# Performance work log

Hardware: AMD Instinct MI355X
Metric: run time of the kernel (lower is better)

The kernel has to match this reference:

```python
import jax, jax.numpy as jnp
import numpy as np

B, S, D_IN, D_OUT = 4, 4096, 1024, 1024

def setup_inputs() -> dict:
    key = jax.random.key(0)
    kx, kq, kk, kv = jax.random.split(key, 4)
    x = jax.random.normal(kx, (B, S, D_IN), dtype=jnp.float32)
    # torch nn.Linear stores weight as [d_out, d_in]; y = x @ W.T
    Wq = jax.random.normal(kq, (D_OUT, D_IN), dtype=jnp.float32) * 0.02
    Wk = jax.random.normal(kk, (D_OUT, D_IN), dtype=jnp.float32) * 0.02
    Wv = jax.random.normal(kv, (D_OUT, D_IN), dtype=jnp.float32) * 0.02
    return {"x": x, "Wq": Wq, "Wk": Wk, "Wv": Wv}

def reference(x, Wq, Wk, Wv):
    b, n, _ = x.shape
    d_out = Wk.shape[0]
    q = jnp.einsum('bnd,od->bno', x, Wq)
    k = jnp.einsum('bnd,od->bno', x, Wk)
    v = jnp.einsum('bnd,od->bno', x, Wv)
    scores = jnp.einsum('bqo,bko->bqk', q, k)  # [B, S, S]
    causal = jnp.triu(jnp.ones((n, n), dtype=bool), k=1)
    scores = jnp.where(causal, -jnp.inf, scores)
    attn = jax.nn.softmax(scores / jnp.sqrt(jnp.float32(d_out)), axis=-1)
    # dropout p=0.0 -> identity
    return jnp.einsum('bqk,bko->bqo', attn, v)
```

## Files before the change

### kernel.cpp

```cpp
#include <hip/hip_runtime.h>


typedef unsigned short u16;
typedef unsigned int u32;
typedef __attribute__((ext_vector_type(8))) short bf16x8;
typedef __attribute__((ext_vector_type(4))) float f32x4;
typedef __attribute__((ext_vector_type(8))) unsigned short u16x8;

__device__ __forceinline__ u16 f2bf(float f) {
  union { float f; unsigned u; } v; v.f = f;
  unsigned r = v.u + 0x7FFFu + ((v.u >> 16) & 1u);
  return (u16)(r >> 16);
}
__device__ __forceinline__ float bf2f(u16 h) {
  union { unsigned u; float f; } v; v.u = ((unsigned)h) << 16;
  return v.f;
}
__device__ __forceinline__ f32x4 mfma16(bf16x8 a, bf16x8 b, f32x4 c) {
  return __builtin_amdgcn_mfma_f32_16x16x32_bf16(a, b, c, 0, 0, 0);
}
__device__ __forceinline__ void gld_lds16(const u16* g, u16* l) {
  __builtin_amdgcn_global_load_lds(
      (const __attribute__((address_space(1))) u32*)g,
      (__attribute__((address_space(3))) u32*)l, 16, 0, 0);
}

__global__ __launch_bounds__(256)
void cast_f32_bf16(const float* __restrict__ src, u16* __restrict__ dst, int n8) {
  int i = blockIdx.x * 256 + threadIdx.x;
  if (i >= n8) return;
  const float4* s4 = (const float4*)src;
  float4 a = s4[2*i], b = s4[2*i+1];
  u16x8 o;
  o[0]=f2bf(a.x); o[1]=f2bf(a.y); o[2]=f2bf(a.z); o[3]=f2bf(a.w);
  o[4]=f2bf(b.x); o[5]=f2bf(b.y); o[6]=f2bf(b.z); o[7]=f2bf(b.w);
  ((u16x8*)dst)[i] = o;
}

__global__ __launch_bounds__(512)
void qkv_gemm(const u16* __restrict__ X, const u16* __restrict__ W,
              u16* __restrict__ Qo, u16* __restrict__ Ko, u16* __restrict__ VTo) {
  __shared__ __align__(16) u16 At[2][256 * 64];
  __shared__ __align__(16) u16 Bt[2][256 * 64];
  const int tid = threadIdx.x;
  const int w = tid >> 6, lane = tid & 63;
  const int g = lane >> 4, c16 = lane & 15;
  const int wr = w >> 2, wc = w & 3;
  const int M0 = blockIdx.x * 256;
  const int N0 = blockIdx.y * 256;

  f32x4 acc[8][4] = {};

  auto stage = [&](int s, int k0) {
#pragma unroll
    for (int i = 0; i < 4; ++i) {
      int ci = i * 512 + tid;
      int r = ci >> 3;
      int c = (ci & 7) ^ (r & 7);
      gld_lds16(X + (size_t)(M0 + r) * 1024 + k0 + c * 8, &At[s][ci * 8]);
    }
#pragma unroll
    for (int i = 0; i < 4; ++i) {
      int ci = i * 512 + tid;
      int r = ci >> 3;
      int c = (ci & 7) ^ (r & 7);
      gld_lds16(W + (size_t)(N0 + r) * 1024 + k0 + c * 8, &Bt[s][ci * 8]);
    }
  };
  auto compute = [&](int s) {
#pragma unroll
    for (int dk = 0; dk < 2; ++dk) {
      bf16x8 af[8], bfr[4];
#pragma unroll
      for (int m = 0; m < 8; ++m) {
        int row = wr * 128 + m * 16 + c16;
        int ch = dk * 4 + g;
        af[m] = *(const bf16x8*)&At[s][row * 64 + ((ch ^ (row & 7)) * 8)];
      }
#pragma unroll
      for (int n = 0; n < 4; ++n) {
        int row = wc * 64 + n * 16 + c16;
        int ch = dk * 4 + g;
        bfr[n] = *(const bf16x8*)&Bt[s][row * 64 + ((ch ^ (row & 7)) * 8)];
      }
#pragma unroll
      for (int m = 0; m < 8; ++m)
#pragma unroll
        for (int n = 0; n < 4; ++n)
          acc[m][n] = mfma16(af[m], bfr[n], acc[m][n]);
    }
  };

  stage(0, 0);
  __syncthreads();
  int cur = 0;
  for (int t = 0; t < 16; ++t) {
    if (t < 15) stage(cur ^ 1, (t + 1) * 64);
    compute(cur);
    __syncthreads();
    cur ^= 1;
  }

  const int which = N0 >> 10;
  const int colbase = N0 & 1023;
#pragma unroll
  for (int m = 0; m < 8; ++m) {
#pragma unroll
    for (int n = 0; n < 4; ++n) {
#pragma unroll
      for (int r = 0; r < 4; ++r) {
        int gm  = M0 + wr * 128 + m * 16 + 4 * g + r;
        int col = colbase + wc * 64 + n * 16 + c16;
        u16 hv = f2bf(acc[m][n][r]);
        if (which == 0) {
          Qo[(size_t)gm * 1024 + col] = hv;
        } else if (which == 1) {
          Ko[(size_t)gm * 1024 + col] = hv;
        } else {
          int b = gm >> 12, s = gm & 4095;
          VTo[((size_t)((b << 10) + col)) * 4096 + s] = hv;
        }
      }
    }
  }
}

__global__ __launch_bounds__(512)
void sgemm_exp(const u16* __restrict__ Q, const u16* __restrict__ K,
               u16* __restrict__ Spack, float* __restrict__ lpart) {
  __shared__ __align__(16) u16 At[2][256 * 64];
  __shared__ __align__(16) u16 Bt[2][256 * 64];
  __shared__ float lsum[256][4];
  const int tid = threadIdx.x;
  const int w = tid >> 6, lane = tid & 63;
  const int g = lane >> 4, c16 = lane & 15;
  const int wr = w >> 2, wc = w & 3;
  const int b = blockIdx.y;

  int L = blockIdx.x, qt = 0;
  while ((qt + 1) * (qt + 2) / 2 <= L) ++qt;
  const int kt = L - qt * (qt + 1) / 2;

  const u16* Qb = Q + (size_t)b * 4096 * 1024 + (size_t)qt * 256 * 1024;
  const u16* Kb = K + (size_t)b * 4096 * 1024 + (size_t)kt * 256 * 1024;

  f32x4 acc[8][4] = {};

  auto stage = [&](int s, int k0) {
#pragma unroll
    for (int i = 0; i < 4; ++i) {
      int ci = i * 512 + tid;
      int r = ci >> 3;
      int c = (ci & 7) ^ (r & 7);
      gld_lds16(Qb + (size_t)r * 1024 + k0 + c * 8, &At[s][ci * 8]);
    }
#pragma unroll
    for (int i = 0; i < 4; ++i) {
      int ci = i * 512 + tid;
      int r = ci >> 3;
      int c = (ci & 7) ^ (r & 7);
      gld_lds16(Kb + (size_t)r * 1024 + k0 + c * 8, &Bt[s][ci * 8]);
    }
  };
  auto compute = [&](int s) {
#pragma unroll
    for (int dk = 0; dk < 2; ++dk) {
      bf16x8 af[8], bfr[4];
#pragma unroll
      for (int m = 0; m < 8; ++m) {
        int row = wr * 128 + m * 16 + c16;
        int ch = dk * 4 + g;
        af[m] = *(const bf16x8*)&At[s][row * 64 + ((ch ^ (row & 7)) * 8)];
      }
#pragma unroll
      for (int n = 0; n < 4; ++n) {
        int row = wc * 64 + n * 16 + c16;
        int ch = dk * 4 + g;
        bfr[n] = *(const bf16x8*)&Bt[s][row * 64 + ((ch ^ (row & 7)) * 8)];
      }
#pragma unroll
      for (int m = 0; m < 8; ++m)
#pragma unroll
        for (int n = 0; n < 4; ++n)
          acc[m][n] = mfma16(af[m], bfr[n], acc[m][n]);
    }
  };

  stage(0, 0);
  __syncthreads();
  int cur = 0;
  for (int t = 0; t < 16; ++t) {
    if (t < 15) stage(cur ^ 1, (t + 1) * 64);
    compute(cur);
    __syncthreads();
    cur ^= 1;
  }

  const int qt128 = 2 * qt + wr;
  const int kt128 = 2 * kt + (wc >> 1);
  const bool exists = (kt128 <= qt128);
  u16* Sb = Spack + (((size_t)b * 528 + (size_t)(qt128 * (qt128 + 1)) / 2 + kt128) << 14);
  const int q0 = qt * 256, k0g = kt * 256;
  float psum[8][4];
#pragma unroll
  for (int m = 0; m < 8; ++m)
#pragma unroll
    for (int r = 0; r < 4; ++r) psum[m][r] = 0.f;
#pragma unroll
  for (int m = 0; m < 8; ++m) {
#pragma unroll
    for (int n = 0; n < 4; ++n) {
#pragma unroll
      for (int r = 0; r < 4; ++r) {
        int rl = wr * 128 + m * 16 + 4 * g + r;
        int cl = wc * 64 + n * 16 + c16;
        float s = acc[m][n][r] * 0.03125f;
        float p = (k0g + cl <= q0 + rl) ? __expf(s) : 0.f;
        u16 pb = f2bf(p);
        if (exists) Sb[(rl & 127) * 128 + (cl & 127)] = pb;
        psum[m][r] += bf2f(pb);
      }
    }
  }
#pragma unroll
  for (int m = 0; m < 8; ++m)
#pragma unroll
    for (int r = 0; r < 4; ++r) {
      float v = psum[m][r];
      v += __shfl_xor(v, 1, 64);
      v += __shfl_xor(v, 2, 64);
      v += __shfl_xor(v, 4, 64);
      v += __shfl_xor(v, 8, 64);
      psum[m][r] = v;
    }
  if (c16 == 0) {
#pragma unroll
    for (int m = 0; m < 8; ++m)
#pragma unroll
      for (int r = 0; r < 4; ++r)
        lsum[wr * 128 + m * 16 + 4 * g + r][wc] = psum[m][r];
  }
  __syncthreads();
  if (tid < 256) {
    float v = lsum[tid][0] + lsum[tid][1] + lsum[tid][2] + lsum[tid][3];
    lpart[((size_t)b * 4096 + q0 + tid) * 16 + kt] = v;
  }
}

__global__ __launch_bounds__(256)
void lreduce(const float* __restrict__ lpart, float* __restrict__ linv) {
  int row = blockIdx.x * 256 + threadIdx.x;
  int nt  = ((row & 4095) >> 8) + 1;
  const float* p = lpart + (size_t)row * 16;
  float s = 0.f;
  for (int i = 0; i < nt; ++i) s += p[i];
  linv[row] = 1.f / s;
}

__global__ __launch_bounds__(512)
void pv_gemm(const u16* __restrict__ Spack, const u16* __restrict__ VT,
             const u16* __restrict__ ztile, const float* __restrict__ linv,
             float* __restrict__ Out) {
  __shared__ __align__(16) u16 At[2][256 * 64];
  __shared__ __align__(16) u16 Bt[2][128 * 64];
  const int tid = threadIdx.x;
  const int w = tid >> 6, lane = tid & 63;
  const int g = lane >> 4, c16 = lane & 15;
  const int wm = w >> 1, wn = w & 1;
  const int p  = blockIdx.x;
  const int d0 = blockIdx.y;
  const int b  = blockIdx.z;

  const u16* Sp_b = Spack + (size_t)b * 528 * 16384;
  const u16* VTb  = VT + (size_t)b * 1024 * 4096;
  float* Ob = Out + (size_t)b * 4096 * 1024;

  for (int pass = 0; pass < 2; ++pass) {
    const int QT = pass == 0 ? p : 15 - p;
    const int M0 = QT * 256;
    const int nsteps = (QT + 1) * 4;
    const int tLo = 2 * QT;
    const size_t triLo = (size_t)(tLo * (tLo + 1)) / 2;
    const size_t triHi = (size_t)((tLo + 1) * (tLo + 2)) / 2;

    f32x4 acc[4][4] = {};

    auto stage = [&](int s, int tt) {
      const int kv0 = tt * 64;
      const int kt128 = tt >> 1;
      const int koff = (tt & 1) * 64;
      const u16* baseLo = (kt128 <= tLo) ? Sp_b + ((triLo + kt128) << 14) : ztile;
      const u16* baseHi = Sp_b + ((triHi + kt128) << 14);
#pragma unroll
      for (int i = 0; i < 4; ++i) {
        int ci = i * 512 + tid;
        int r = ci >> 3;
        int c = (ci & 7) ^ (r & 7);
        const u16* base = (i < 2) ? baseLo : baseHi;
        gld_lds16(base + (size_t)(r & 127) * 128 + koff + c * 8, &At[s][ci * 8]);
      }
#pragma unroll
      for (int i = 0; i < 2; ++i) {
        int ci = i * 512 + tid;
        int r = ci >> 3;
        int c = (ci & 7) ^ (r & 7);
        gld_lds16(VTb + (size_t)(d0 * 128 + r) * 4096 + kv0 + c * 8, &Bt[s][ci * 8]);
      }
    };
    auto compute = [&](int s) {
#pragma unroll
      for (int dk = 0; dk < 2; ++dk) {
        bf16x8 af[4], bfr[4];
#pragma unroll
        for (int m = 0; m < 4; ++m) {
          int row = wm * 64 + m * 16 + c16;
          int ch = dk * 4 + g;
          af[m] = *(const bf16x8*)&At[s][row * 64 + ((ch ^ (row & 7)) * 8)];
        }
#pragma unroll
        for (int n = 0; n < 4; ++n) {
          int row = wn * 64 + n * 16 + c16;
          int ch = dk * 4 + g;
          bfr[n] = *(const bf16x8*)&Bt[s][row * 64 + ((ch ^ (row & 7)) * 8)];
        }
#pragma unroll
        for (int m = 0; m < 4; ++m)
#pragma unroll
          for (int n = 0; n < 4; ++n)
            acc[m][n] = mfma16(af[m], bfr[n], acc[m][n]);
      }
    };

    stage(0, 0);
    __syncthreads();
    int cur = 0;
    for (int t = 0; t < nsteps; ++t) {
      if (t + 1 < nsteps) stage(cur ^ 1, t + 1);
      compute(cur);
      __syncthreads();
      cur ^= 1;
    }

    const float* lb = linv + (size_t)b * 4096 + M0;
#pragma unroll
    for (int m = 0; m < 4; ++m) {
#pragma unroll
      for (int r = 0; r < 4; ++r) {
        int rl = wm * 64 + m * 16 + 4 * g + r;
        float li = lb[rl];
#pragma unroll
        for (int n = 0; n < 4; ++n) {
          int dcol = d0 * 128 + wn * 64 + n * 16 + c16;
          Ob[(size_t)(M0 + rl) * 1024 + dcol] = acc[m][n][r] * li;
        }
      }
    }
  }
}

__global__ __launch_bounds__(512, 2)
void attn_kernel(const u16* __restrict__ Q, const u16* __restrict__ K,
                 const u16* __restrict__ VT, float* __restrict__ Out) {
  __shared__ u16 kv_lds[32 * 1024];
  __shared__ float s_part[4][32][33];
  __shared__ u16 p_lds[32 * 40];
  __shared__ float l_lds[32];

  const int tid = threadIdx.x;
  const int w = tid >> 6, lane = tid & 63;
  const int g = lane >> 4, c16 = lane & 15;
  const int b  = blockIdx.x & 3;
  const int qb = 127 - (blockIdx.x >> 2);
  const int qs = qb * 32;
  const int kh = w & 1, dq = w >> 1;

  const u16* Qb  = Q  + (size_t)b * 4096 * 1024;
  const u16* Kb  = K  + (size_t)b * 4096 * 1024;
  const u16* VTb = VT + (size_t)b * 1024 * 4096;

  bf16x8 qfrag[2][8];
#pragma unroll
  for (int qh = 0; qh < 2; ++qh)
#pragma unroll
    for (int dk = 0; dk < 8; ++dk)
      qfrag[qh][dk] = *(const bf16x8*)(Qb + (size_t)(qs + qh * 16 + c16) * 1024
                                       + dq * 256 + dk * 32 + g * 8);

  f32x4 oacc[2][8] = {};
  if (tid < 32) l_lds[tid] = 0.f;

  const int qrow_p = tid >> 4;
  const int kk     = tid & 15;
  const int gq     = qs + qrow_p;

  for (int j = 0; j <= qb; ++j) {
    const int kv0 = j * 32;
    __syncthreads();
    uint4 rk[8];
#pragma unroll
    for (int i = 0; i < 8; ++i) {
      int ci = i * 512 + tid;
      int r  = ci >> 7;
      int c  = (ci & 127) ^ (r & 7);
      rk[i] = *(const uint4*)(Kb + (size_t)(kv0 + r) * 1024 + c * 8);
    }
#pragma unroll
    for (int i = 0; i < 8; ++i)
      *(uint4*)&kv_lds[(size_t)(i * 512 + tid) * 8] = rk[i];
    __syncthreads();
    f32x4 sacc[2] = {};
#pragma unroll
    for (int dk = 0; dk < 8; ++dk) {
      int kvrow = kh * 16 + c16;
      int ch    = dq * 32 + dk * 4 + g;
      bf16x8 kf = *(const bf16x8*)&kv_lds[kvrow * 1024 + ((ch ^ (kvrow & 7)) * 8)];
      sacc[0] = mfma16(qfrag[0][dk], kf, sacc[0]);
      sacc[1] = mfma16(qfrag[1][dk], kf, sacc[1]);
    }
#pragma unroll
    for (int qh = 0; qh < 2; ++qh)
#pragma unroll
      for (int r = 0; r < 4; ++r)
        s_part[dq][qh * 16 + 4 * g + r][kh * 16 + c16] = sacc[qh][r];
    __syncthreads();
    uint4 rv[8];
#pragma unroll
    for (int i = 0; i < 8; ++i) {
      int ci = i * 512 + tid;
      int d  = ((ci >> 6) << 4) + (ci & 15);
      int c  = (ci >> 4) & 3;
      rv[i] = *(const uint4*)(VTb + (size_t)d * 4096 + kv0 + c * 8);
    }
    {
      float psum = 0.f;
#pragma unroll
      for (int h = 0; h < 2; ++h) {
        int kcol = kk + h * 16;
        float s = s_part[0][qrow_p][kcol] + s_part[1][qrow_p][kcol]
                + s_part[2][qrow_p][kcol] + s_part[3][qrow_p][kcol];
        s *= 0.03125f;
        float p = (kv0 + kcol <= gq) ? __expf(s) : 0.f;
        u16 pb = f2bf(p);
        p_lds[qrow_p * 40 + kcol] = pb;
        psum += bf2f(pb);
      }
#pragma unroll
      for (int off = 1; off < 16; off <<= 1)
        psum += __shfl_xor(psum, off, 64);
      if (kk == 0) l_lds[qrow_p] += psum;
    }
#pragma unroll
    for (int i = 0; i < 8; ++i)
      *(uint4*)&kv_lds[(size_t)(i * 512 + tid) * 8] = rv[i];
    __syncthreads();
    bf16x8 pa0 = *(const bf16x8*)&p_lds[(0  + c16) * 40 + g * 8];
    bf16x8 pa1 = *(const bf16x8*)&p_lds[(16 + c16) * 40 + g * 8];
#pragma unroll
    for (int f = 0; f < 8; ++f) {
      int dcol = w * 128 + f * 16 + c16;
      int pos  = (dcol >> 4) * 64 + g * 16 + (dcol & 15);
      bf16x8 vf = *(const bf16x8*)&kv_lds[(size_t)pos * 8];
      oacc[0][f] = mfma16(pa0, vf, oacc[0][f]);
      oacc[1][f] = mfma16(pa1, vf, oacc[1][f]);
    }
  }

  float* Ob = Out + (size_t)b * 4096 * 1024;
#pragma unroll
  for (int qh = 0; qh < 2; ++qh) {
#pragma unroll
    for (int r = 0; r < 4; ++r) {
      int ql = qh * 16 + 4 * g + r;
      float linvv = 1.f / l_lds[ql];
#pragma unroll
      for (int f = 0; f < 8; ++f)
        Ob[(size_t)(qs + ql) * 1024 + w * 128 + f * 16 + c16] = oacc[qh][f][r] * linvv;
    }
  }
}

extern "C" void kernel_launch(void* const* d_in, const int* in_sizes, int n_in,
                              void* d_out, int out_size, void* d_ws, size_t ws_size,
                              hipStream_t stream) {
  const float* x  = (const float*)d_in[0];
  const float* Wq = (const float*)d_in[1];
  const float* Wk = (const float*)d_in[2];
  const float* Wv = (const float*)d_in[3];
  float* out = (float*)d_out;

  u16* ws    = (u16*)d_ws;
  u16* wWqkv = ws;
  u16* wX    = wWqkv + (size_t)3 * 1024 * 1024;
  u16* wQ    = wX + (size_t)16384 * 1024;
  u16* wK    = wQ + (size_t)16384 * 1024;
  u16* wVT   = wK + (size_t)16384 * 1024;
  u16* wSp   = wVT + (size_t)16384 * 1024;
  float* lpart = (float*)(ws + (size_t)104857600);
  float* linv  = (float*)(ws + (size_t)105906176);

  cast_f32_bf16<<<dim3(8192), 256, 0, stream>>>(x, wX, 16777216 / 8);
  cast_f32_bf16<<<dim3(512), 256, 0, stream>>>(Wq, wWqkv,                 1048576 / 8);
  cast_f32_bf16<<<dim3(512), 256, 0, stream>>>(Wk, wWqkv + 1048576,       1048576 / 8);
  cast_f32_bf16<<<dim3(512), 256, 0, stream>>>(Wv, wWqkv + 2 * 1048576,   1048576 / 8);

  qkv_gemm<<<dim3(64, 12), 512, 0, stream>>>(wX, wWqkv, wQ, wK, wVT);

  if (ws_size >= (size_t)211877888) {
    hipMemsetAsync(wX, 0, 32768, stream);
    sgemm_exp<<<dim3(136, 4), 512, 0, stream>>>(wQ, wK, wSp, lpart);
    lreduce<<<dim3(64), 256, 0, stream>>>(lpart, linv);
    pv_gemm<<<dim3(8, 8, 4), 512, 0, stream>>>(wSp, wVT, wX, linv, out);
  } else {
    attn_kernel<<<dim3(512), 512, 0, stream>>>(wQ, wK, wVT, out);
  }
}
```

Baseline: 393.6 us.

## Use 4-stage 32-wide K pipeline with fragment-ordered LDS layout in GEMMs

Replaces the double-buffered 64-wide K stages in all three GEMM kernels with a 4-slot ring of 32-wide K stages. Each slot is laid out in MFMA-fragment order with an XOR swizzle, so each fragment read is a single contiguous vector load. Partial vmcnt waits let three stages of global-to-LDS loads stay in flight, and s_setprio raises wave priority around the MFMA block. This is meant to hide memory latency better, at the cost of twice as many barriers per K and hand-tuned vmcnt counts that must match the number of loads issued.

```diff
diff --git a/kernel.cpp b/kernel.cpp
--- a/kernel.cpp
+++ b/kernel.cpp
@@ -40,8 +40,8 @@
 __global__ __launch_bounds__(512)
 void qkv_gemm(const u16* __restrict__ X, const u16* __restrict__ W,
               u16* __restrict__ Qo, u16* __restrict__ Ko, u16* __restrict__ VTo) {
-  __shared__ __align__(16) u16 At[2][256 * 64];
-  __shared__ __align__(16) u16 Bt[2][256 * 64];
+  __shared__ __align__(16) u16 LA[4][8192];
+  __shared__ __align__(16) u16 LB[4][8192];
   const int tid = threadIdx.x;
   const int w = tid >> 6, lane = tid & 63;
   const int g = lane >> 4, c16 = lane & 15;
@@ -50,55 +50,61 @@
   const int N0 = blockIdx.y * 256;
 
   f32x4 acc[8][4] = {};
-
-  auto stage = [&](int s, int k0) {
-#pragma unroll
-    for (int i = 0; i < 4; ++i) {
-      int ci = i * 512 + tid;
-      int r = ci >> 3;
-      int c = (ci & 7) ^ (r & 7);
-      gld_lds16(X + (size_t)(M0 + r) * 1024 + k0 + c * 8, &At[s][ci * 8]);
-    }
-#pragma unroll
-    for (int i = 0; i < 4; ++i) {
-      int ci = i * 512 + tid;
-      int r = ci >> 3;
-      int c = (ci & 7) ^ (r & 7);
-      gld_lds16(W + (size_t)(N0 + r) * 1024 + k0 + c * 8, &Bt[s][ci * 8]);
+  const int roff = c16 * 32 + ((g ^ (c16 & 3)) * 8);
+
+  auto stage = [&](int s) {
+    const int slot = s & 3;
+    const int k0 = s * 32;
+#pragma unroll
+    for (int i = 0; i < 2; ++i) {
+      int p = i * 512 + tid;
+      int r = ((p >> 6) << 4) | ((p >> 2) & 15);
+      int c = (p & 3) ^ ((p >> 2) & 3);
+      gld_lds16(X + (size_t)(M0 + r) * 1024 + k0 + c * 8, &LA[slot][p * 8]);
+    }
+#pragma unroll
+    for (int i = 0; i < 2; ++i) {
+      int p = i * 512 + tid;
+      int r = ((p >> 6) << 4) | ((p >> 2) & 15);
+      int c = (p & 3) ^ ((p >> 2) & 3);
+      gld_lds16(W + (size_t)(N0 + r) * 1024 + k0 + c * 8, &LB[slot][p * 8]);
     }
   };
-  auto compute = [&](int s) {
-#pragma unroll
-    for (int dk = 0; dk < 2; ++dk) {
-      bf16x8 af[8], bfr[4];
-#pragma unroll
-      for (int m = 0; m < 8; ++m) {
-        int row = wr * 128 + m * 16 + c16;
-        int ch = dk * 4 + g;
-        af[m] = *(const bf16x8*)&At[s][row * 64 + ((ch ^ (row & 7)) * 8)];
-      }
-#pragma unroll
-      for (int n = 0; n < 4; ++n) {
-        int row = wc * 64 + n * 16 + c16;
-        int ch = dk * 4 + g;
-        bfr[n] = *(const bf16x8*)&Bt[s][row * 64 + ((ch ^ (row & 7)) * 8)];
-      }
+
+  stage(0); stage(1); stage(2);
+  for (int s = 0; s < 32; ++s) {
+    if (s + 3 < 32) {
+      stage(s + 3);
+      asm volatile("s_waitcnt vmcnt(12)" ::: "memory");
+    } else {
+      asm volatile("s_waitcnt vmcnt(0)" ::: "memory");
+    }
+    __builtin_amdgcn_sched_barrier(0);
+    __builtin_amdgcn_s_barrier();
+    __builtin_amdgcn_sched_barrier(0);
+    {
+      const int slot = s & 3;
+      const u16* A = LA[slot];
+      const u16* B = LB[slot];
+      bf16x8 af[8], bf[4];
 #pragma unroll
       for (int m = 0; m < 8; ++m)
+        af[m] = *(const bf16x8*)&A[(wr * 8 + m) * 512 + roff];
+#pragma unroll
+      for (int n = 0; n < 4; ++n)
+        bf[n] = *(const bf16x8*)&B[(wc * 4 + n) * 512 + roff];
+      __builtin_amdgcn_s_setprio(1);
+#pragma unroll
+      for (int m = 0; m < 8; ++m)
 #pragma unroll
         for (int n = 0; n < 4; ++n)
-          acc[m][n] = mfma16(af[m], bfr[n], acc[m][n]);
-    }
-  };
-
-  stage(0, 0);
-  __syncthreads();
-  int cur = 0;
-  for (int t = 0; t < 16; ++t) {
-    if (t < 15) stage(cur ^ 1, (t + 1) * 64);
-    compute(cur);
-    __syncthreads();
-    cur ^= 1;
+          acc[m][n] = mfma16(af[m], bf[n], acc[m][n]);
+      __builtin_amdgcn_s_setprio(0);
+    }
+    asm volatile("s_waitcnt lgkmcnt(0)" ::: "memory");
+    __builtin_amdgcn_sched_barrier(0);
+    __builtin_amdgcn_s_barrier();
+    __builtin_amdgcn_sched_barrier(0);
   }
 
   const int which = N0 >> 10;
@@ -117,8 +123,8 @@
         } else if (which == 1) {
           Ko[(size_t)gm * 1024 + col] = hv;
         } else {
-          int b = gm >> 12, s = gm & 4095;
-          VTo[((size_t)((b << 10) + col)) * 4096 + s] = hv;
+          int b = gm >> 12, s2 = gm & 4095;
+          VTo[((size_t)((b << 10) + col)) * 4096 + s2] = hv;
         }
       }
     }
@@ -128,8 +134,8 @@
 __global__ __launch_bounds__(512)
 void sgemm_exp(const u16* __restrict__ Q, const u16* __restrict__ K,
                u16* __restrict__ Spack, float* __restrict__ lpart) {
-  __shared__ __align__(16) u16 At[2][256 * 64];
-  __shared__ __align__(16) u16 Bt[2][256 * 64];
+  __shared__ __align__(16) u16 LA[4][8192];
+  __shared__ __align__(16) u16 LB[4][8192];
   __shared__ float lsum[256][4];
   const int tid = threadIdx.x;
   const int w = tid >> 6, lane = tid & 63;
@@ -145,55 +151,61 @@
   const u16* Kb = K + (size_t)b * 4096 * 1024 + (size_t)kt * 256 * 1024;
 
   f32x4 acc[8][4] = {};
-
-  auto stage = [&](int s, int k0) {
-#pragma unroll
-    for (int i = 0; i < 4; ++i) {
-      int ci = i * 512 + tid;
-      int r = ci >> 3;
-      int c = (ci & 7) ^ (r & 7);
-      gld_lds16(Qb + (size_t)r * 1024 + k0 + c * 8, &At[s][ci * 8]);
-    }
-#pragma unroll
-    for (int i = 0; i < 4; ++i) {
-      int ci = i * 512 + tid;
-      int r = ci >> 3;
-      int c = (ci & 7) ^ (r & 7);
-      gld_lds16(Kb + (size_t)r * 1024 + k0 + c * 8, &Bt[s][ci * 8]);
+  const int roff = c16 * 32 + ((g ^ (c16 & 3)) * 8);
+
+  auto stage = [&](int s) {
+    const int slot = s & 3;
+    const int k0 = s * 32;
+#pragma unroll
+    for (int i = 0; i < 2; ++i) {
+      int p = i * 512 + tid;
+      int r = ((p >> 6) << 4) | ((p >> 2) & 15);
+      int c = (p & 3) ^ ((p >> 2) & 3);
+      gld_lds16(Qb + (size_t)r * 1024 + k0 + c * 8, &LA[slot][p * 8]);
+    }
+#pragma unroll
+    for (int i = 0; i < 2; ++i) {
+      int p = i * 512 + tid;
+      int r = ((p >> 6) << 4) | ((p >> 2) & 15);
+      int c = (p & 3) ^ ((p >> 2) & 3);
+      gld_lds16(Kb + (size_t)r * 1024 + k0 + c * 8, &LB[slot][p * 8]);
     }
   };
-  auto compute = [&](int s) {
-#pragma unroll
-    for (int dk = 0; dk < 2; ++dk) {
-      bf16x8 af[8], bfr[4];
-#pragma unroll
-      for (int m = 0; m < 8; ++m) {
-        int row = wr * 128 + m * 16 + c16;
-        int ch = dk * 4 + g;
-        af[m] = *(const bf16x8*)&At[s][row * 64 + ((ch ^ (row & 7)) * 8)];
-      }
-#pragma unroll
-      for (int n = 0; n < 4; ++n) {
-        int row = wc * 64 + n * 16 + c16;
-        int ch = dk * 4 + g;
-        bfr[n] = *(const bf16x8*)&Bt[s][row * 64 + ((ch ^ (row & 7)) * 8)];
-      }
+
+  stage(0); stage(1); stage(2);
+  for (int s = 0; s < 32; ++s) {
+    if (s + 3 < 32) {
+      stage(s + 3);
+      asm volatile("s_waitcnt vmcnt(12)" ::: "memory");
+    } else {
+      asm volatile("s_waitcnt vmcnt(0)" ::: "memory");
+    }
+    __builtin_amdgcn_sched_barrier(0);
+    __builtin_amdgcn_s_barrier();
+    __builtin_amdgcn_sched_barrier(0);
+    {
+      const int slot = s & 3;
+      const u16* A = LA[slot];
+      const u16* B = LB[slot];
+      bf16x8 af[8], bf[4];
 #pragma unroll
       for (int m = 0; m < 8; ++m)
+        af[m] = *(const bf16x8*)&A[(wr * 8 + m) * 512 + roff];
+#pragma unroll
+      for (int n = 0; n < 4; ++n)
+        bf[n] = *(const bf16x8*)&B[(wc * 4 + n) * 512 + roff];
+      __builtin_amdgcn_s_setprio(1);
+#pragma unroll
+      for (int m = 0; m < 8; ++m)
 #pragma unroll
         for (int n = 0; n < 4; ++n)
-          acc[m][n] = mfma16(af[m], bfr[n], acc[m][n]);
-    }
-  };
-
-  stage(0, 0);
-  __syncthreads();
-  int cur = 0;
-  for (int t = 0; t < 16; ++t) {
-    if (t < 15) stage(cur ^ 1, (t + 1) * 64);
-    compute(cur);
-    __syncthreads();
-    cur ^= 1;
+          acc[m][n] = mfma16(af[m], bf[n], acc[m][n]);
+      __builtin_amdgcn_s_setprio(0);
+    }
+    asm volatile("s_waitcnt lgkmcnt(0)" ::: "memory");
+    __builtin_amdgcn_sched_barrier(0);
+    __builtin_amdgcn_s_barrier();
+    __builtin_amdgcn_sched_barrier(0);
   }
 
   const int qt128 = 2 * qt + wr;
@@ -261,84 +273,87 @@
 void pv_gemm(const u16* __restrict__ Spack, const u16* __restrict__ VT,
              const u16* __restrict__ ztile, const float* __restrict__ linv,
              float* __restrict__ Out) {
-  __shared__ __align__(16) u16 At[2][256 * 64];
-  __shared__ __align__(16) u16 Bt[2][128 * 64];
+  __shared__ __align__(16) u16 LA[4][8192];
+  __shared__ __align__(16) u16 LB[4][4096];
   const int tid = threadIdx.x;
   const int w = tid >> 6, lane = tid & 63;
   const int g = lane >> 4, c16 = lane & 15;
   const int wm = w >> 1, wn = w & 1;
-  const int p  = blockIdx.x;
+  const int pp = blockIdx.x;
   const int d0 = blockIdx.y;
   const int b  = blockIdx.z;
 
   const u16* Sp_b = Spack + (size_t)b * 528 * 16384;
   const u16* VTb  = VT + (size_t)b * 1024 * 4096;
   float* Ob = Out + (size_t)b * 4096 * 1024;
+  const int roff = c16 * 32 + ((g ^ (c16 & 3)) * 8);
 
   for (int pass = 0; pass < 2; ++pass) {
-    const int QT = pass == 0 ? p : 15 - p;
+    const int QT = pass == 0 ? pp : 15 - pp;
     const int M0 = QT * 256;
-    const int nsteps = (QT + 1) * 4;
+    const int nsub = (QT + 1) * 8;
     const int tLo = 2 * QT;
     const size_t triLo = (size_t)(tLo * (tLo + 1)) / 2;
     const size_t triHi = (size_t)((tLo + 1) * (tLo + 2)) / 2;
 
     f32x4 acc[4][4] = {};
 
-    auto stage = [&](int s, int tt) {
-      const int kv0 = tt * 64;
-      const int kt128 = tt >> 1;
-      const int koff = (tt & 1) * 64;
+    auto stage = [&](int s) {
+      const int slot = s & 3;
+      const int kt128 = s >> 2;
+      const int koff = (s & 3) * 32;
       const u16* baseLo = (kt128 <= tLo) ? Sp_b + ((triLo + kt128) << 14) : ztile;
       const u16* baseHi = Sp_b + ((triHi + kt128) << 14);
 #pragma unroll
-      for (int i = 0; i < 4; ++i) {
-        int ci = i * 512 + tid;
-        int r = ci >> 3;
-        int c = (ci & 7) ^ (r & 7);
-        const u16* base = (i < 2) ? baseLo : baseHi;
-        gld_lds16(base + (size_t)(r & 127) * 128 + koff + c * 8, &At[s][ci * 8]);
-      }
-#pragma unroll
       for (int i = 0; i < 2; ++i) {
-        int ci = i * 512 + tid;
-        int r = ci >> 3;
-        int c = (ci & 7) ^ (r & 7);
-        gld_lds16(VTb + (size_t)(d0 * 128 + r) * 4096 + kv0 + c * 8, &Bt[s][ci * 8]);
+        int p = i * 512 + tid;
+        int r = ((p >> 6) << 4) | ((p >> 2) & 15);
+        int c = (p & 3) ^ ((p >> 2) & 3);
+        const u16* base = i ? baseHi : baseLo;
+        gld_lds16(base + (size_t)(r & 127) * 128 + koff + c * 8, &LA[slot][p * 8]);
+      }
+      {
+        int p = tid;
+        int r = ((p >> 6) << 4) | ((p >> 2) & 15);
+        int c = (p & 3) ^ ((p >> 2) & 3);
+        gld_lds16(VTb + (size_t)(d0 * 128 + r) * 4096 + s * 32 + c * 8, &LB[slot][p * 8]);
       }
     };
-    auto compute = [&](int s) {
-#pragma unroll
-      for (int dk = 0; dk < 2; ++dk) {
-        bf16x8 af[4], bfr[4];
-#pragma unroll
-        for (int m = 0; m < 4; ++m) {
-          int row = wm * 64 + m * 16 + c16;
-          int ch = dk * 4 + g;
-          af[m] = *(const bf16x8*)&At[s][row * 64 + ((ch ^ (row & 7)) * 8)];
-        }
-#pragma unroll
-        for (int n = 0; n < 4; ++n) {
-          int row = wn * 64 + n * 16 + c16;
-          int ch = dk * 4 + g;
-          bfr[n] = *(const bf16x8*)&Bt[s][row * 64 + ((ch ^ (row & 7)) * 8)];
-        }
+
+    stage(0); stage(1); stage(2);
+    for (int s = 0; s < nsub; ++s) {
+      if (s + 3 < nsub) {
+        stage(s + 3);
+        asm volatile("s_waitcnt vmcnt(9)" ::: "memory");
+      } else {
+        asm volatile("s_waitcnt vmcnt(0)" ::: "memory");
+      }
+      __builtin_amdgcn_sched_barrier(0);
+      __builtin_amdgcn_s_barrier();
+      __builtin_amdgcn_sched_barrier(0);
+      {
+        const int slot = s & 3;
+        const u16* A = LA[slot];
+        const u16* B = LB[slot];
+        bf16x8 af[4], bf[4];
 #pragma unroll
         for (int m = 0; m < 4; ++m)
+          af[m] = *(const bf16x8*)&A[(wm * 4 + m) * 512 + roff];
+#pragma unroll
+        for (int n = 0; n < 4; ++n)
+          bf[n] = *(const bf16x8*)&B[(wn * 4 + n) * 512 + roff];
+        __builtin_amdgcn_s_setprio(1);
+#pragma unroll
+        for (int m = 0; m < 4; ++m)
 #pragma unroll
           for (int n = 0; n < 4; ++n)
-            acc[m][n] = mfma16(af[m], bfr[n], acc[m][n]);
-      }
-    };
-
-    stage(0, 0);
-    __syncthreads();
-    int cur = 0;
-    for (int t = 0; t < nsteps; ++t) {
-      if (t + 1 < nsteps) stage(cur ^ 1, t + 1);
-      compute(cur);
-      __syncthreads();
-      cur ^= 1;
+            acc[m][n] = mfma16(af[m], bf[n], acc[m][n]);
+        __builtin_amdgcn_s_setprio(0);
+      }
+      asm volatile("s_waitcnt lgkmcnt(0)" ::: "memory");
+      __builtin_amdgcn_sched_barrier(0);
+      __builtin_amdgcn_s_barrier();
+      __builtin_amdgcn_sched_barrier(0);
     }
 
     const float* lb = linv + (size_t)b * 4096 + M0;
```

Measured after the change: 462.3 us. 1.17x slower.

## Restructure GEMM main loops with explicit vmcnt waits, phased barriers and setprio

Applied to the files above, without the earlier changes.

Rewrites the K-loop of the QKV, QK^T and PV GEMMs so the next tile's global-to-LDS loads are issued first. Each wave then waits with an explicit s_waitcnt vmcnt only for the current buffer's loads, not all outstanding ones, before a raw s_barrier. The MFMA block is split into phases: A fragments are loaded in halves, MFMAs are wrapped in s_setprio, and an LDS-wait-plus-barrier closes each phase, aiming to interleave waves' LDS reads and matrix ops and to ease register pressure. The cost is several extra workgroup barriers per K step, and correctness now depends on the hand-counted vmcnt values matching the number of issued loads.

```diff
diff --git a/kernel.cpp b/kernel.cpp
--- a/kernel.cpp
+++ b/kernel.cpp
@@ -24,6 +24,12 @@
       (const __attribute__((address_space(1))) u32*)g,
       (__attribute__((address_space(3))) u32*)l, 16, 0, 0);
 }
+#define PHASE_END() do {                                   \
+    asm volatile("s_waitcnt lgkmcnt(0)" ::: "memory");     \
+    __builtin_amdgcn_sched_barrier(0);                     \
+    __builtin_amdgcn_s_barrier();                          \
+    __builtin_amdgcn_sched_barrier(0);                     \
+  } while (0)
 
 __global__ __launch_bounds__(256)
 void cast_f32_bf16(const float* __restrict__ src, u16* __restrict__ dst, int n8) {
@@ -67,38 +73,57 @@
       gld_lds16(W + (size_t)(N0 + r) * 1024 + k0 + c * 8, &Bt[s][ci * 8]);
     }
   };
-  auto compute = [&](int s) {
+
+  stage(0, 0);
+  for (int t = 0; t < 16; ++t) {
+    const int buf = t & 1;
+    if (t < 15) {
+      stage(buf ^ 1, (t + 1) * 64);
+      asm volatile("s_waitcnt vmcnt(8)" ::: "memory");
+    } else {
+      asm volatile("s_waitcnt vmcnt(0)" ::: "memory");
+    }
+    __builtin_amdgcn_sched_barrier(0);
+    __builtin_amdgcn_s_barrier();
+    __builtin_amdgcn_sched_barrier(0);
+    const u16* A = At[buf];
+    const u16* B = Bt[buf];
 #pragma unroll
     for (int dk = 0; dk < 2; ++dk) {
-      bf16x8 af[8], bfr[4];
-#pragma unroll
-      for (int m = 0; m < 8; ++m) {
-        int row = wr * 128 + m * 16 + c16;
-        int ch = dk * 4 + g;
-        af[m] = *(const bf16x8*)&At[s][row * 64 + ((ch ^ (row & 7)) * 8)];
-      }
+      const int ch = dk * 4 + g;
+      bf16x8 bfr[4], af[4];
 #pragma unroll
       for (int n = 0; n < 4; ++n) {
         int row = wc * 64 + n * 16 + c16;
-        int ch = dk * 4 + g;
-        bfr[n] = *(const bf16x8*)&Bt[s][row * 64 + ((ch ^ (row & 7)) * 8)];
-      }
-#pragma unroll
-      for (int m = 0; m < 8; ++m)
+        bfr[n] = *(const bf16x8*)&B[row * 64 + ((ch ^ (row & 7)) * 8)];
+      }
+#pragma unroll
+      for (int m = 0; m < 4; ++m) {
+        int row = wr * 128 + m * 16 + c16;
+        af[m] = *(const bf16x8*)&A[row * 64 + ((ch ^ (row & 7)) * 8)];
+      }
+      __builtin_amdgcn_s_setprio(1);
+#pragma unroll
+      for (int m = 0; m < 4; ++m)
 #pragma unroll
         for (int n = 0; n < 4; ++n)
           acc[m][n] = mfma16(af[m], bfr[n], acc[m][n]);
-    }
-  };
-
-  stage(0, 0);
-  __syncthreads();
-  int cur = 0;
-  for (int t = 0; t < 16; ++t) {
-    if (t < 15) stage(cur ^ 1, (t + 1) * 64);
-    compute(cur);
-    __syncthreads();
-    cur ^= 1;
+      __builtin_amdgcn_s_setprio(0);
+      PHASE_END();
+#pragma unroll
+      for (int m = 0; m < 4; ++m) {
+        int row = wr * 128 + (m + 4) * 16 + c16;
+        af[m] = *(const bf16x8*)&A[row * 64 + ((ch ^ (row & 7)) * 8)];
+      }
+      __builtin_amdgcn_s_setprio(1);
+#pragma unroll
+      for (int m = 0; m < 4; ++m)
+#pragma unroll
+        for (int n = 0; n < 4; ++n)
+          acc[m + 4][n] = mfma16(af[m], bfr[n], acc[m + 4][n]);
+      __builtin_amdgcn_s_setprio(0);
+      PHASE_END();
+    }
   }
 
   const int which = N0 >> 10;
@@ -117,8 +142,8 @@
         } else if (which == 1) {
           Ko[(size_t)gm * 1024 + col] = hv;
         } else {
-          int b = gm >> 12, s = gm & 4095;
-          VTo[((size_t)((b << 10) + col)) * 4096 + s] = hv;
+          int b = gm >> 12, s2 = gm & 4095;
+          VTo[((size_t)((b << 10) + col)) * 4096 + s2] = hv;
         }
       }
     }
@@ -162,38 +187,57 @@
       gld_lds16(Kb + (size_t)r * 1024 + k0 + c * 8, &Bt[s][ci * 8]);
     }
   };
-  auto compute = [&](int s) {
+
+  stage(0, 0);
+  for (int t = 0; t < 16; ++t) {
+    const int buf = t & 1;
+    if (t < 15) {
+      stage(buf ^ 1, (t + 1) * 64);
+      asm volatile("s_waitcnt vmcnt(8)" ::: "memory");
+    } else {
+      asm volatile("s_waitcnt vmcnt(0)" ::: "memory");
+    }
+    __builtin_amdgcn_sched_barrier(0);
+    __builtin_amdgcn_s_barrier();
+    __builtin_amdgcn_sched_barrier(0);
+    const u16* A = At[buf];
+    const u16* B = Bt[buf];
 #pragma unroll
     for (int dk = 0; dk < 2; ++dk) {
-      bf16x8 af[8], bfr[4];
-#pragma unroll
-      for (int m = 0; m < 8; ++m) {
-        int row = wr * 128 + m * 16 + c16;
-        int ch = dk * 4 + g;
-        af[m] = *(const bf16x8*)&At[s][row * 64 + ((ch ^ (row & 7)) * 8)];
-      }
+      const int ch = dk * 4 + g;
+      bf16x8 bfr[4], af[4];
 #pragma unroll
       for (int n = 0; n < 4; ++n) {
         int row = wc * 64 + n * 16 + c16;
-        int ch = dk * 4 + g;
-        bfr[n] = *(const bf16x8*)&Bt[s][row * 64 + ((ch ^ (row & 7)) * 8)];
-      }
-#pragma unroll
-      for (int m = 0; m < 8; ++m)
+        bfr[n] = *(const bf16x8*)&B[row * 64 + ((ch ^ (row & 7)) * 8)];
+      }
+#pragma unroll
+      for (int m = 0; m < 4; ++m) {
+        int row = wr * 128 + m * 16 + c16;
+        af[m] = *(const bf16x8*)&A[row * 64 + ((ch ^ (row & 7)) * 8)];
+      }
+      __builtin_amdgcn_s_setprio(1);
+#pragma unroll
+      for (int m = 0; m < 4; ++m)
 #pragma unroll
         for (int n = 0; n < 4; ++n)
           acc[m][n] = mfma16(af[m], bfr[n], acc[m][n]);
-    }
-  };
-
-  stage(0, 0);
-  __syncthreads();
-  int cur = 0;
-  for (int t = 0; t < 16; ++t) {
-    if (t < 15) stage(cur ^ 1, (t + 1) * 64);
-    compute(cur);
-    __syncthreads();
-    cur ^= 1;
+      __builtin_amdgcn_s_setprio(0);
+      PHASE_END();
+#pragma unroll
+      for (int m = 0; m < 4; ++m) {
+        int row = wr * 128 + (m + 4) * 16 + c16;
+        af[m] = *(const bf16x8*)&A[row * 64 + ((ch ^ (row & 7)) * 8)];
+      }
+      __builtin_amdgcn_s_setprio(1);
+#pragma unroll
+      for (int m = 0; m < 4; ++m)
+#pragma unroll
+        for (int n = 0; n < 4; ++n)
+          acc[m + 4][n] = mfma16(af[m], bfr[n], acc[m + 4][n]);
+      __builtin_amdgcn_s_setprio(0);
+      PHASE_END();
+    }
   }
 
   const int qt128 = 2 * qt + wr;
@@ -267,7 +311,7 @@
   const int w = tid >> 6, lane = tid & 63;
   const int g = lane >> 4, c16 = lane & 15;
   const int wm = w >> 1, wn = w & 1;
-  const int p  = blockIdx.x;
+  const int pp = blockIdx.x;
   const int d0 = blockIdx.y;
   const int b  = blockIdx.z;
 
@@ -276,7 +320,7 @@
   float* Ob = Out + (size_t)b * 4096 * 1024;
 
   for (int pass = 0; pass < 2; ++pass) {
-    const int QT = pass == 0 ? p : 15 - p;
+    const int QT = pass == 0 ? pp : 15 - pp;
     const int M0 = QT * 256;
     const int nsteps = (QT + 1) * 4;
     const int tLo = 2 * QT;
@@ -307,38 +351,44 @@
         gld_lds16(VTb + (size_t)(d0 * 128 + r) * 4096 + kv0 + c * 8, &Bt[s][ci * 8]);
       }
     };
-    auto compute = [&](int s) {
+
+    stage(0, 0);
+    for (int t = 0; t < nsteps; ++t) {
+      const int buf = t & 1;
+      if (t + 1 < nsteps) {
+        stage(buf ^ 1, t + 1);
+        asm volatile("s_waitcnt vmcnt(6)" ::: "memory");
+      } else {
+        asm volatile("s_waitcnt vmcnt(0)" ::: "memory");
+      }
+      __builtin_amdgcn_sched_barrier(0);
+      __builtin_amdgcn_s_barrier();
+      __builtin_amdgcn_sched_barrier(0);
+      const u16* A = At[buf];
+      const u16* B = Bt[buf];
 #pragma unroll
       for (int dk = 0; dk < 2; ++dk) {
+        const int ch = dk * 4 + g;
         bf16x8 af[4], bfr[4];
 #pragma unroll
         for (int m = 0; m < 4; ++m) {
           int row = wm * 64 + m * 16 + c16;
-          int ch = dk * 4 + g;
-          af[m] = *(const bf16x8*)&At[s][row * 64 + ((ch ^ (row & 7)) * 8)];
+          af[m] = *(const bf16x8*)&A[row * 64 + ((ch ^ (row & 7)) * 8)];
         }
 #pragma unroll
         for (int n = 0; n < 4; ++n) {
           int row = wn * 64 + n * 16 + c16;
-          int ch = dk * 4 + g;
-          bfr[n] = *(const bf16x8*)&Bt[s][row * 64 + ((ch ^ (row & 7)) * 8)];
+          bfr[n] = *(const bf16x8*)&B[row * 64 + ((ch ^ (row & 7)) * 8)];
         }
+        __builtin_amdgcn_s_setprio(1);
 #pragma unroll
         for (int m = 0; m < 4; ++m)
 #pragma unroll
           for (int n = 0; n < 4; ++n)
             acc[m][n] = mfma16(af[m], bfr[n], acc[m][n]);
-      }
-    };
-
-    stage(0, 0);
-    __syncthreads();
-    int cur = 0;
-    for (int t = 0; t < nsteps; ++t) {
-      if (t + 1 < nsteps) stage(cur ^ 1, t + 1);
-      compute(cur);
-      __syncthreads();
-      cur ^= 1;
+        __builtin_amdgcn_s_setprio(0);
+        PHASE_END();
+      }
     }
 
     const float* lb = linv + (size_t)b * 4096 + M0;
```

Measured after the change: 407.1 us. +3.4%, slower.

## Replace GEMM mainloop with fine-grained 8-phase ping-pong pipeline in QKV and score kernels

Applied to the files above, without the earlier changes.

Replaces the simple double-buffered stage/compute loop in the QKV projection and QK^T score kernels with a shared macro. The macro splits each 256x64 tile into 128-row halves and interleaves half-tile global-to-LDS prefetches with quarter-tile MFMA groups. It uses explicit s_barrier, lgkmcnt/vmcnt waits, sched_barrier and s_setprio to overlap memory traffic with matrix math. The point is to hide load latency and keep MFMA units busy, at the cost of many more barriers and fragile hand-placed wait counts. Both kernels also get launch_bounds with min 1 block per SM so the compiler has more registers available.

```diff
diff --git a/kernel.cpp b/kernel.cpp
--- a/kernel.cpp
+++ b/kernel.cpp
@@ -24,6 +24,11 @@
       (const __attribute__((address_space(1))) u32*)g,
       (__attribute__((address_space(3))) u32*)l, 16, 0, 0);
 }
+#define BAR() __builtin_amdgcn_s_barrier()
+#define LGKM0() do { asm volatile("s_waitcnt lgkmcnt(0)" ::: "memory"); \
+                     __builtin_amdgcn_sched_barrier(0); } while (0)
+#define VMCNT2() asm volatile("s_waitcnt vmcnt(2)" ::: "memory")
+#define VMCNT0() asm volatile("s_waitcnt vmcnt(0)" ::: "memory")
 
 __global__ __launch_bounds__(256)
 void cast_f32_bf16(const float* __restrict__ src, u16* __restrict__ dst, int n8) {
@@ -37,69 +42,135 @@
   ((u16x8*)dst)[i] = o;
 }
 
-__global__ __launch_bounds__(512)
+#define GEMM8_CORE(Abase, Bbase)                                              \
+  auto stageA = [&](int bufi, int h, int t) {                                 \
+    _Pragma("unroll")                                                         \
+    for (int i = 0; i < 2; ++i) {                                             \
+      int ci = i * 512 + tid;                                                 \
+      int r  = ci >> 3;                                                       \
+      int c  = (ci & 7) ^ (r & 7);                                            \
+      gld_lds16(Abase + (size_t)(h * 128 + r) * 1024 + t * 64 + c * 8,        \
+                &At[bufi][h][ci * 8]);                                        \
+    }                                                                         \
+  };                                                                          \
+  auto stageB = [&](int bufi, int h, int t) {                                 \
+    _Pragma("unroll")                                                         \
+    for (int i = 0; i < 2; ++i) {                                             \
+      int ci = i * 512 + tid;                                                 \
+      int r  = ci >> 3;                                                       \
+      int c  = (ci & 7) ^ (r & 7);                                            \
+      gld_lds16(Bbase + (size_t)(h * 128 + r) * 1024 + t * 64 + c * 8,        \
+                &Bt[bufi][h][ci * 8]);                                        \
+    }                                                                         \
+  };                                                                          \
+  bf16x8 af[4][2], bfr[2][2];                                                 \
+  auto readA = [&](int bufi, int mb) {                                        \
+    _Pragma("unroll")                                                         \
+    for (int m = 0; m < 4; ++m)                                               \
+      _Pragma("unroll")                                                       \
+      for (int dk = 0; dk < 2; ++dk) {                                        \
+        int r  = (mb + m) * 16 + c16;                                         \
+        int ch = dk * 4 + g;                                                  \
+        af[m][dk] = *(const bf16x8*)&At[bufi][wr][r * 64 + ((ch ^ (r & 7)) * 8)]; \
+      }                                                                       \
+  };                                                                          \
+  auto readB = [&](int bufi, int nb) {                                        \
+    _Pragma("unroll")                                                         \
+    for (int n = 0; n < 2; ++n)                                               \
+      _Pragma("unroll")                                                       \
+      for (int dk = 0; dk < 2; ++dk) {                                        \
+        int r  = (wc & 1) * 64 + (nb + n) * 16 + c16;                         \
+        int ch = dk * 4 + g;                                                  \
+        bfr[n][dk] = *(const bf16x8*)&Bt[bufi][wc >> 1][r * 64 + ((ch ^ (r & 7)) * 8)]; \
+      }                                                                       \
+  };                                                                          \
+  auto domfma = [&](int mb, int nb) {                                         \
+    __builtin_amdgcn_s_setprio(1);                                            \
+    _Pragma("unroll")                                                         \
+    for (int dk = 0; dk < 2; ++dk)                                            \
+      _Pragma("unroll")                                                       \
+      for (int m = 0; m < 4; ++m)                                             \
+        _Pragma("unroll")                                                     \
+        for (int n = 0; n < 2; ++n)                                           \
+          acc[mb + m][nb + n] = mfma16(af[m][dk], bfr[n][dk], acc[mb + m][nb + n]); \
+    __builtin_amdgcn_s_setprio(0);                                            \
+  };                                                                          \
+                \
+  stageB(0, 0, 0); stageB(0, 1, 0); stageA(0, 0, 0); stageA(0, 1, 0);         \
+  stageB(1, 0, 1);                                                            \
+  VMCNT2();                                                                   \
+  BAR();                                                                      \
+  for (int it = 0; it < 8; ++it) {                                            \
+    const bool pf = (it < 7);                                                 \
+    const int t1 = 2 * it + 1, t2 = 2 * it + 2, t3 = 2 * it + 3;              \
+                                               \
+    readA(0, 0); readB(0, 0);                                                 \
+    stageB(1, 1, t1);                                                         \
+    BAR(); LGKM0();                                                           \
+    domfma(0, 0);                                                             \
+    BAR();                                                                    \
+                                                    \
+    readA(0, 4);                                                              \
+    stageA(1, 0, t1);                                                         \
+    BAR(); LGKM0();                                                           \
+    domfma(4, 0);                                                             \
+    BAR();                                                                    \
+                                                    \
+    readB(0, 2);                                                              \
+    stageA(1, 1, t1);                                                         \
+    BAR(); LGKM0();                                                           \
+    domfma(4, 2);                                                             \
+    BAR();                                                                    \
+                                    \
+    readA(0, 0);                                                              \
+    if (pf) stageB(0, 0, t2);                                                 \
+    BAR(); LGKM0();                                                           \
+    domfma(0, 2);                                                             \
+    if (pf) { VMCNT2(); } else { VMCNT0(); }                                  \
+    BAR();                                                                    \
+                                                             \
+    readA(1, 0); readB(1, 0);                                                 \
+    if (pf) stageB(0, 1, t2);                                                 \
+    BAR(); LGKM0();                                                           \
+    domfma(0, 0);                                                             \
+    BAR();                                                                    \
+                                                                  \
+    readA(1, 4);                                                              \
+    if (pf) stageA(0, 0, t2);                                                 \
+    BAR(); LGKM0();                                                           \
+    domfma(4, 0);                                                             \
+    BAR();                                                                    \
+                                                                  \
+    readB(1, 2);                                                              \
+    if (pf) stageA(0, 1, t2);                                                 \
+    BAR(); LGKM0();                                                           \
+    domfma(4, 2);                                                             \
+    BAR();                                                                    \
+                                                  \
+    readA(1, 0);                                                              \
+    if (pf) stageB(1, 0, t3);                                                 \
+    BAR(); LGKM0();                                                           \
+    domfma(0, 2);                                                             \
+    if (pf) { VMCNT2(); } else { VMCNT0(); }                                  \
+    BAR();                                                                    \
+  }
+
+__global__ __launch_bounds__(512, 1)
 void qkv_gemm(const u16* __restrict__ X, const u16* __restrict__ W,
               u16* __restrict__ Qo, u16* __restrict__ Ko, u16* __restrict__ VTo) {
-  __shared__ __align__(16) u16 At[2][256 * 64];
-  __shared__ __align__(16) u16 Bt[2][256 * 64];
+  __shared__ __align__(16) u16 At[2][2][128 * 64];
+  __shared__ __align__(16) u16 Bt[2][2][128 * 64];
   const int tid = threadIdx.x;
   const int w = tid >> 6, lane = tid & 63;
   const int g = lane >> 4, c16 = lane & 15;
   const int wr = w >> 2, wc = w & 3;
   const int M0 = blockIdx.x * 256;
   const int N0 = blockIdx.y * 256;
+  const u16* Abase = X + (size_t)M0 * 1024;
+  const u16* Bbase = W + (size_t)N0 * 1024;
 
   f32x4 acc[8][4] = {};
-
-  auto stage = [&](int s, int k0) {
-#pragma unroll
-    for (int i = 0; i < 4; ++i) {
-      int ci = i * 512 + tid;
-      int r = ci >> 3;
-      int c = (ci & 7) ^ (r & 7);
-      gld_lds16(X + (size_t)(M0 + r) * 1024 + k0 + c * 8, &At[s][ci * 8]);
-    }
-#pragma unroll
-    for (int i = 0; i < 4; ++i) {
-      int ci = i * 512 + tid;
-      int r = ci >> 3;
-      int c = (ci & 7) ^ (r & 7);
-      gld_lds16(W + (size_t)(N0 + r) * 1024 + k0 + c * 8, &Bt[s][ci * 8]);
-    }
-  };
-  auto compute = [&](int s) {
-#pragma unroll
-    for (int dk = 0; dk < 2; ++dk) {
-      bf16x8 af[8], bfr[4];
-#pragma unroll
-      for (int m = 0; m < 8; ++m) {
-        int row = wr * 128 + m * 16 + c16;
-        int ch = dk * 4 + g;
-        af[m] = *(const bf16x8*)&At[s][row * 64 + ((ch ^ (row & 7)) * 8)];
-      }
-#pragma unroll
-      for (int n = 0; n < 4; ++n) {
-        int row = wc * 64 + n * 16 + c16;
-        int ch = dk * 4 + g;
-        bfr[n] = *(const bf16x8*)&Bt[s][row * 64 + ((ch ^ (row & 7)) * 8)];
-      }
-#pragma unroll
-      for (int m = 0; m < 8; ++m)
-#pragma unroll
-        for (int n = 0; n < 4; ++n)
-          acc[m][n] = mfma16(af[m], bfr[n], acc[m][n]);
-    }
-  };
-
-  stage(0, 0);
-  __syncthreads();
-  int cur = 0;
-  for (int t = 0; t < 16; ++t) {
-    if (t < 15) stage(cur ^ 1, (t + 1) * 64);
-    compute(cur);
-    __syncthreads();
-    cur ^= 1;
-  }
+  GEMM8_CORE(Abase, Bbase);
 
   const int which = N0 >> 10;
   const int colbase = N0 & 1023;
@@ -117,19 +188,19 @@
         } else if (which == 1) {
           Ko[(size_t)gm * 1024 + col] = hv;
         } else {
-          int b = gm >> 12, s = gm & 4095;
-          VTo[((size_t)((b << 10) + col)) * 4096 + s] = hv;
+          int b = gm >> 12, s2 = gm & 4095;
+          VTo[((size_t)((b << 10) + col)) * 4096 + s2] = hv;
         }
       }
     }
   }
 }
 
-__global__ __launch_bounds__(512)
+__global__ __launch_bounds__(512, 1)
 void sgemm_exp(const u16* __restrict__ Q, const u16* __restrict__ K,
                u16* __restrict__ Spack, float* __restrict__ lpart) {
-  __shared__ __align__(16) u16 At[2][256 * 64];
-  __shared__ __align__(16) u16 Bt[2][256 * 64];
+  __shared__ __align__(16) u16 At[2][2][128 * 64];
+  __shared__ __align__(16) u16 Bt[2][2][128 * 64];
   __shared__ float lsum[256][4];
   const int tid = threadIdx.x;
   const int w = tid >> 6, lane = tid & 63;
@@ -141,60 +212,11 @@
   while ((qt + 1) * (qt + 2) / 2 <= L) ++qt;
   const int kt = L - qt * (qt + 1) / 2;
 
-  const u16* Qb = Q + (size_t)b * 4096 * 1024 + (size_t)qt * 256 * 1024;
-  const u16* Kb = K + (size_t)b * 4096 * 1024 + (size_t)kt * 256 * 1024;
+  const u16* Abase = Q + (size_t)b * 4096 * 1024 + (size_t)qt * 256 * 1024;
+  const u16* Bbase = K + (size_t)b * 4096 * 1024 + (size_t)kt * 256 * 1024;
 
   f32x4 acc[8][4] = {};
-
-  auto stage = [&](int s, int k0) {
-#pragma unroll
-    for (int i = 0; i < 4; ++i) {
-      int ci = i * 512 + tid;
-      int r = ci >> 3;
-      int c = (ci & 7) ^ (r & 7);
-      gld_lds16(Qb + (size_t)r * 1024 + k0 + c * 8, &At[s][ci * 8]);
-    }
-#pragma unroll
-    for (int i = 0; i < 4; ++i) {
-      int ci = i * 512 + tid;
-      int r = ci >> 3;
-      int c = (ci & 7) ^ (r & 7);
-      gld_lds16(Kb + (size_t)r * 1024 + k0 + c * 8, &Bt[s][ci * 8]);
-    }
-  };
-  auto compute = [&](int s) {
-#pragma unroll
-    for (int dk = 0; dk < 2; ++dk) {
-      bf16x8 af[8], bfr[4];
-#pragma unroll
-      for (int m = 0; m < 8; ++m) {
-        int row = wr * 128 + m * 16 + c16;
-        int ch = dk * 4 + g;
-        af[m] = *(const bf16x8*)&At[s][row * 64 + ((ch ^ (row & 7)) * 8)];
-      }
-#pragma unroll
-      for (int n = 0; n < 4; ++n) {
-        int row = wc * 64 + n * 16 + c16;
-        int ch = dk * 4 + g;
-        bfr[n] = *(const bf16x8*)&Bt[s][row * 64 + ((ch ^ (row & 7)) * 8)];
-      }
-#pragma unroll
-      for (int m = 0; m < 8; ++m)
-#pragma unroll
-        for (int n = 0; n < 4; ++n)
-          acc[m][n] = mfma16(af[m], bfr[n], acc[m][n]);
-    }
-  };
-
-  stage(0, 0);
-  __syncthreads();
-  int cur = 0;
-  for (int t = 0; t < 16; ++t) {
-    if (t < 15) stage(cur ^ 1, (t + 1) * 64);
-    compute(cur);
-    __syncthreads();
-    cur ^= 1;
-  }
+  GEMM8_CORE(Abase, Bbase);
 
   const int qt128 = 2 * qt + wr;
   const int kt128 = 2 * kt + (wc >> 1);
@@ -267,7 +289,7 @@
   const int w = tid >> 6, lane = tid & 63;
   const int g = lane >> 4, c16 = lane & 15;
   const int wm = w >> 1, wn = w & 1;
-  const int p  = blockIdx.x;
+  const int pp = blockIdx.x;
   const int d0 = blockIdx.y;
   const int b  = blockIdx.z;
 
@@ -276,7 +298,7 @@
   float* Ob = Out + (size_t)b * 4096 * 1024;
 
   for (int pass = 0; pass < 2; ++pass) {
-    const int QT = pass == 0 ? p : 15 - p;
+    const int QT = pass == 0 ? pp : 15 - pp;
     const int M0 = QT * 256;
     const int nsteps = (QT + 1) * 4;
     const int tLo = 2 * QT;
@@ -310,24 +332,24 @@
     auto compute = [&](int s) {
 #pragma unroll
       for (int dk = 0; dk < 2; ++dk) {
-        bf16x8 af[4], bfr[4];
+        bf16x8 af2[4], bf2[4];
 #pragma unroll
         for (int m = 0; m < 4; ++m) {
           int row = wm * 64 + m * 16 + c16;
           int ch = dk * 4 + g;
-          af[m] = *(const bf16x8*)&At[s][row * 64 + ((ch ^ (row & 7)) * 8)];
+          af2[m] = *(const bf16x8*)&At[s][row * 64 + ((ch ^ (row & 7)) * 8)];
         }
 #pragma unroll
         for (int n = 0; n < 4; ++n) {
           int row = wn * 64 + n * 16 + c16;
           int ch = dk * 4 + g;
-          bfr[n] = *(const bf16x8*)&Bt[s][row * 64 + ((ch ^ (row & 7)) * 8)];
+          bf2[n] = *(const bf16x8*)&Bt[s][row * 64 + ((ch ^ (row & 7)) * 8)];
         }
 #pragma unroll
         for (int m = 0; m < 4; ++m)
 #pragma unroll
           for (int n = 0; n < 4; ++n)
-            acc[m][n] = mfma16(af[m], bfr[n], acc[m][n]);
+            acc[m][n] = mfma16(af2[m], bf2[n], acc[m][n]);
       }
     };
 
```

After: 398.7 us. About the same (+1.3%).
